# Performance work log

Measured on AMD Instinct MI355X. Metric: run time of the kernel, lower is better.

Reference implementation:

```python
import jax, jax.numpy as jnp
import numpy as np

N_VOCAB = 100000
N_FIELDS = 40
K = 64
ATTN = 64
BATCH = 2048

def setup_inputs() -> dict:
    key = jax.random.key(0)
    ks = jax.random.split(key, 9)
    x = jax.random.randint(ks[0], (BATCH, N_FIELDS), 0, N_VOCAB)
    lin_table = jax.random.normal(ks[1], (N_VOCAB, 1), dtype=jnp.float32) * 0.01
    V_table = jax.random.normal(ks[2], (N_VOCAB, K), dtype=jnp.float32) * 0.01
    W1 = jax.random.normal(ks[3], (K, ATTN), dtype=jnp.float32) * (1.0 / np.sqrt(K))
    b1 = jnp.zeros((ATTN,), dtype=jnp.float32)
    W2 = jax.random.normal(ks[4], (ATTN, 1), dtype=jnp.float32) * (1.0 / np.sqrt(ATTN))
    b2 = jnp.zeros((1,), dtype=jnp.float32)
    Wf = jax.random.normal(ks[5], (K, 1), dtype=jnp.float32) * (1.0 / np.sqrt(K))
    bf = jnp.zeros((1,), dtype=jnp.float32)
    return {"x": x, "lin_table": lin_table, "V_table": V_table,
            "W1": W1, "b1": b1, "W2": W2, "b2": b2, "Wf": Wf, "bf": bf}

def reference(x, lin_table, V_table, W1, b1, W2, b2, Wf, bf):
    # linear part: sum of per-feature scalar weights -> [B, 1]
    linear_part = jnp.sum(lin_table[x], axis=1)
    # embeddings: [B, F, K]
    embd = V_table[x]
    # pairwise interactions: [B, F, F, K]
    pw = embd[:, :, None, :] * embd[:, None, :, :]
    # attention MLP: k -> attn -> 1, scores [B, F, F, 1]
    h = jax.nn.relu(jnp.einsum('bijk,ka->bija', pw, W1) + b1)
    scores = jnp.einsum('bija,ao->bijo', h, W2) + b2
    # softmax over dim=2 (second field axis)
    probs = jax.nn.softmax(scores, axis=2)
    # weighted sum over j then i -> [B, K]
    weighted = jnp.sum(probs * pw, axis=2)
    weighted_embd = jnp.sum(weighted, axis=1)
    interaction_part = weighted_embd @ Wf + bf  # [B, 1]
    return jax.nn.sigmoid(linear_part + interaction_part)[:, 0]
```

## Files before the change

kernel.cpp:

```cpp
#include <hip/hip_runtime.h>

#define NF 40
#define KD 64

typedef float f32x4 __attribute__((ext_vector_type(4)));
typedef _Float16 f16x8 __attribute__((ext_vector_type(8)));
typedef _Float16 f16x4 __attribute__((ext_vector_type(4)));

__global__ __launch_bounds__(256, 4)
void afm_kernel(const int* __restrict__ x,
                const float* __restrict__ lin_table,
                const float* __restrict__ V_table,
                const float* __restrict__ W1,
                const float* __restrict__ b1,
                const float* __restrict__ W2,
                const float* __restrict__ b2,
                const float* __restrict__ Wf,
                const float* __restrict__ bf,
                float* __restrict__ out)
{
    __shared__ _Float16 e16[NF][72];
    __shared__ _Float16 eT16[KD][72];
    __shared__ _Float16 Q16[48][72];
    __shared__ unsigned short lut[832];
    __shared__ float wsum[4];

    const int b = blockIdx.x;
    const int tid = threadIdx.x;
    const int w = tid >> 6;
    const int lane = tid & 63;
    const int l15 = lane & 15;
    const int lhi = lane >> 4;

    {
        f16x8 zh = {0, 0, 0, 0, 0, 0, 0, 0};
        for (int t = tid; t < 48 * 72 / 8; t += 256)
            reinterpret_cast<f16x8*>(&Q16[0][0])[t] = zh;
        int r = tid >> 2, c8 = tid & 3;
        *reinterpret_cast<f16x8*>(&eT16[r][40 + 8 * c8]) = zh;
    }
    for (int p0 = tid; p0 < 832; p0 += 256) {
        int p = p0 > 819 ? 819 : p0;
        int i = (int)((81.0f - sqrtf(6561.0f - 8.0f * (float)p)) * 0.5f);
        int off = (i * (81 - i)) >> 1;
        if ((((i + 1) * (80 - i)) >> 1) <= p) { ++i; off = (i * (81 - i)) >> 1; }
        else if (off > p)                     { --i; off = (i * (81 - i)) >> 1; }
        lut[p0] = (unsigned short)((i << 8) | (i + (p - off)));
    }

    for (int q = tid; q < NF * (KD / 4); q += 256) {
        int i = q >> 4, k4 = q & 15;
        int ix = x[b * NF + i];
        float4 v = reinterpret_cast<const float4*>(V_table + (size_t)ix * KD)[k4];
        f16x4 hv = {(_Float16)v.x, (_Float16)v.y, (_Float16)v.z, (_Float16)v.w};
        *reinterpret_cast<f16x4*>(&e16[i][k4 * 4]) = hv;
        eT16[k4 * 4 + 0][i] = hv[0];
        eT16[k4 * 4 + 1][i] = hv[1];
        eT16[k4 * 4 + 2][i] = hv[2];
        eT16[k4 * 4 + 3][i] = hv[3];
    }
    float linv = (w == 0 && lane < NF) ? lin_table[x[b * NF + lane]] : 0.0f;

    f16x8 Af[4][2];
    #pragma unroll
    for (int at = 0; at < 4; ++at) {
        #pragma unroll
        for (int ks = 0; ks < 2; ++ks) {
            f16x8 t;
            #pragma unroll
            for (int el = 0; el < 8; ++el)
                t[el] = (_Float16)W1[(ks * 32 + lhi * 8 + el) * KD + at * 16 + l15];
            Af[at][ks] = t;
        }
    }
    f32x4 b1v[4], w2v[4];
    #pragma unroll
    for (int at = 0; at < 4; ++at) {
        b1v[at] = *reinterpret_cast<const f32x4*>(b1 + at * 16 + lhi * 4);
        w2v[at] = *reinterpret_cast<const f32x4*>(W2 + at * 16 + lhi * 4);
    }
    const float wfv = Wf[w * 16 + l15];
    const float bf0 = bf[0];
    __syncthreads();

    const int k0 = lhi * 8;
    for (int mt = w; mt < 52; mt += 4) {
        const int v = lut[mt * 16 + l15];
        const int i = v >> 8;
        const int j = v & 255;
        const _Float16* ei = &e16[i][0];
        const _Float16* ej = &e16[j][0];
        f16x8 B0 = (*reinterpret_cast<const f16x8*>(ei + k0)) *
                   (*reinterpret_cast<const f16x8*>(ej + k0));
        f16x8 B1 = (*reinterpret_cast<const f16x8*>(ei + k0 + 32)) *
                   (*reinterpret_cast<const f16x8*>(ej + k0 + 32));

        f32x4 d[4];
        #pragma unroll
        for (int at = 0; at < 4; ++at) {
            d[at] = b1v[at];
            d[at] = __builtin_amdgcn_mfma_f32_16x16x32_f16(Af[at][0], B0, d[at], 0, 0, 0);
            d[at] = __builtin_amdgcn_mfma_f32_16x16x32_f16(Af[at][1], B1, d[at], 0, 0, 0);
        }
        float s = 0.0f;
        #pragma unroll
        for (int at = 0; at < 4; ++at) {
            #pragma unroll
            for (int r = 0; r < 4; ++r)
                s = fmaf(fmaxf(d[at][r], 0.0f), w2v[at][r], s);
        }
        s += __shfl_xor(s, 16, 64);
        s += __shfl_xor(s, 32, 64);
        float qv = __expf(s);
        if (lhi == 0) {
            _Float16 qh = (_Float16)qv;
            Q16[i][j] = qh;
            Q16[j][i] = qh;
        }
    }
    __syncthreads();

    const int c = w * 16 + l15;
    const f16x8 bv0 = *reinterpret_cast<const f16x8*>(&eT16[c][lhi * 8]);
    const f16x8 bv1 = *reinterpret_cast<const f16x8*>(&eT16[c][32 + lhi * 8]);
    f16x8 one0, one1;
    #pragma unroll
    for (int el = 0; el < 8; ++el) {
        one0[el] = (_Float16)1.0f;
        one1[el] = (lhi == 0) ? (_Float16)1.0f : (_Float16)0.0f;
    }

    float acc = 0.0f;
    #pragma unroll
    for (int mt = 0; mt < 3; ++mt) {
        const _Float16* qrow = &Q16[mt * 16 + l15][0];
        f16x8 aq0 = *reinterpret_cast<const f16x8*>(qrow + lhi * 8);
        f16x8 aq1 = *reinterpret_cast<const f16x8*>(qrow + 32 + lhi * 8);

        f32x4 dz = {0.f, 0.f, 0.f, 0.f};
        dz = __builtin_amdgcn_mfma_f32_16x16x32_f16(aq0, one0, dz, 0, 0, 0);
        dz = __builtin_amdgcn_mfma_f32_16x16x32_f16(aq1, one1, dz, 0, 0, 0);

        f32x4 dq = {0.f, 0.f, 0.f, 0.f};
        dq = __builtin_amdgcn_mfma_f32_16x16x32_f16(aq0, bv0, dq, 0, 0, 0);
        dq = __builtin_amdgcn_mfma_f32_16x16x32_f16(aq1, bv1, dq, 0, 0, 0);

        f16x4 ev4 = *reinterpret_cast<const f16x4*>(&eT16[c][mt * 16 + lhi * 4]);
        #pragma unroll
        for (int r = 0; r < 4; ++r) {
            int ii = mt * 16 + lhi * 4 + r;
            float rz = (ii < NF) ? __builtin_amdgcn_rcpf(dz[r]) : 0.0f;
            acc = fmaf((float)ev4[r] * dq[r], rz, acc);
        }
    }

    acc += __shfl_xor(acc, 16, 64);
    acc += __shfl_xor(acc, 32, 64);
    float ip = acc * wfv;
    ip += __shfl_xor(ip, 1, 64);
    ip += __shfl_xor(ip, 2, 64);
    ip += __shfl_xor(ip, 4, 64);
    ip += __shfl_xor(ip, 8, 64);
    if (lane == 0) wsum[w] = ip;
    __syncthreads();

    if (w == 0) {
        linv += __shfl_xor(linv, 32, 64);
        linv += __shfl_xor(linv, 16, 64);
        linv += __shfl_xor(linv, 8, 64);
        linv += __shfl_xor(linv, 4, 64);
        linv += __shfl_xor(linv, 2, 64);
        linv += __shfl_xor(linv, 1, 64);
        if (lane == 0) {
            float z = linv + wsum[0] + wsum[1] + wsum[2] + wsum[3] + bf0;
            out[b] = 1.0f / (1.0f + __expf(-z));
        }
    }
}

extern "C" void kernel_launch(void* const* d_in, const int* in_sizes, int n_in,
                              void* d_out, int out_size, void* d_ws, size_t ws_size,
                              hipStream_t stream) {
    const int*   x         = (const int*)d_in[0];
    const float* lin_table = (const float*)d_in[1];
    const float* V_table   = (const float*)d_in[2];
    const float* W1        = (const float*)d_in[3];
    const float* b1        = (const float*)d_in[4];
    const float* W2        = (const float*)d_in[5];
    const float* b2        = (const float*)d_in[6];
    const float* Wf        = (const float*)d_in[7];
    const float* bf        = (const float*)d_in[8];
    float* out = (float*)d_out;

    const int batch = in_sizes[0] / NF;
    afm_kernel<<<batch, 256, 0, stream>>>(x, lin_table, V_table, W1, b1, W2, b2,
                                          Wf, bf, out);
}
```

Before: 32.61 us.

## Process two samples per block and overlap second gather with first scoring

```diff
diff --git a/kernel.cpp b/kernel.cpp
--- a/kernel.cpp
+++ b/kernel.cpp
@@ -19,25 +19,28 @@
                 const float* __restrict__ bf,
                 float* __restrict__ out)
 {
-    __shared__ _Float16 e16[NF][72];
-    __shared__ _Float16 eT16[KD][72];
+    __shared__ _Float16 eA[2][NF][72];
+    __shared__ _Float16 eT[2][KD][72];
     __shared__ _Float16 Q16[48][72];
     __shared__ unsigned short lut[832];
     __shared__ float wsum[4];
 
-    const int b = blockIdx.x;
     const int tid = threadIdx.x;
     const int w = tid >> 6;
     const int lane = tid & 63;
     const int l15 = lane & 15;
     const int lhi = lane >> 4;
+    const int s0 = blockIdx.x * 2;
+    const int s1 = s0 + 1;
 
     {
         f16x8 zh = {0, 0, 0, 0, 0, 0, 0, 0};
-        for (int t = tid; t < 48 * 72 / 8; t += 256)
+        for (int t = tid; t < 432; t += 256)
             reinterpret_cast<f16x8*>(&Q16[0][0])[t] = zh;
-        int r = tid >> 2, c8 = tid & 3;
-        *reinterpret_cast<f16x8*>(&eT16[r][40 + 8 * c8]) = zh;
+        for (int t = tid; t < 512; t += 256) {
+            int s = t >> 8, r = (t >> 2) & 63, c8 = t & 3;
+            *reinterpret_cast<f16x8*>(&eT[s][r][40 + 8 * c8]) = zh;
+        }
     }
     for (int p0 = tid; p0 < 832; p0 += 256) {
         int p = p0 > 819 ? 819 : p0;
@@ -48,18 +51,20 @@
         lut[p0] = (unsigned short)((i << 8) | (i + (p - off)));
     }
 
-    for (int q = tid; q < NF * (KD / 4); q += 256) {
-        int i = q >> 4, k4 = q & 15;
-        int ix = x[b * NF + i];
-        float4 v = reinterpret_cast<const float4*>(V_table + (size_t)ix * KD)[k4];
-        f16x4 hv = {(_Float16)v.x, (_Float16)v.y, (_Float16)v.z, (_Float16)v.w};
-        *reinterpret_cast<f16x4*>(&e16[i][k4 * 4]) = hv;
-        eT16[k4 * 4 + 0][i] = hv[0];
-        eT16[k4 * 4 + 1][i] = hv[1];
-        eT16[k4 * 4 + 2][i] = hv[2];
-        eT16[k4 * 4 + 3][i] = hv[3];
-    }
-    float linv = (w == 0 && lane < NF) ? lin_table[x[b * NF + lane]] : 0.0f;
+    auto gather = [&](int smp, int s) -> float {
+        for (int q = tid; q < NF * (KD / 4); q += 256) {
+            int i = q >> 4, k4 = q & 15;
+            int ix = x[smp * NF + i];
+            float4 v = reinterpret_cast<const float4*>(V_table + (size_t)ix * KD)[k4];
+            f16x4 hv = {(_Float16)v.x, (_Float16)v.y, (_Float16)v.z, (_Float16)v.w};
+            *reinterpret_cast<f16x4*>(&eA[s][i][k4 * 4]) = hv;
+            eT[s][k4 * 4 + 0][i] = hv[0];
+            eT[s][k4 * 4 + 1][i] = hv[1];
+            eT[s][k4 * 4 + 2][i] = hv[2];
+            eT[s][k4 * 4 + 3][i] = hv[3];
+        }
+        return (w == 0 && lane < NF) ? lin_table[x[smp * NF + lane]] : 0.0f;
+    };
 
     f16x8 Af[4][2];
     #pragma unroll
@@ -81,90 +86,88 @@
     }
     const float wfv = Wf[w * 16 + l15];
     const float bf0 = bf[0];
-    __syncthreads();
-
     const int k0 = lhi * 8;
-    for (int mt = w; mt < 52; mt += 4) {
-        const int v = lut[mt * 16 + l15];
-        const int i = v >> 8;
-        const int j = v & 255;
-        const _Float16* ei = &e16[i][0];
-        const _Float16* ej = &e16[j][0];
-        f16x8 B0 = (*reinterpret_cast<const f16x8*>(ei + k0)) *
-                   (*reinterpret_cast<const f16x8*>(ej + k0));
-        f16x8 B1 = (*reinterpret_cast<const f16x8*>(ei + k0 + 32)) *
-                   (*reinterpret_cast<const f16x8*>(ej + k0 + 32));
-
-        f32x4 d[4];
+
+    auto score = [&](int s) {
+        for (int mt = w; mt < 52; mt += 4) {
+            const int v = lut[mt * 16 + l15];
+            const int i = v >> 8;
+            const int j = v & 255;
+            const _Float16* ei = &eA[s][i][0];
+            const _Float16* ej = &eA[s][j][0];
+            f16x8 B0 = (*reinterpret_cast<const f16x8*>(ei + k0)) *
+                       (*reinterpret_cast<const f16x8*>(ej + k0));
+            f16x8 B1 = (*reinterpret_cast<const f16x8*>(ei + k0 + 32)) *
+                       (*reinterpret_cast<const f16x8*>(ej + k0 + 32));
+            f32x4 d[4];
+            #pragma unroll
+            for (int at = 0; at < 4; ++at) {
+                d[at] = b1v[at];
+                d[at] = __builtin_amdgcn_mfma_f32_16x16x32_f16(Af[at][0], B0, d[at], 0, 0, 0);
+                d[at] = __builtin_amdgcn_mfma_f32_16x16x32_f16(Af[at][1], B1, d[at], 0, 0, 0);
+            }
+            float sacc = 0.0f;
+            #pragma unroll
+            for (int at = 0; at < 4; ++at) {
+                #pragma unroll
+                for (int r = 0; r < 4; ++r)
+                    sacc = fmaf(fmaxf(d[at][r], 0.0f), w2v[at][r], sacc);
+            }
+            sacc += __shfl_xor(sacc, 16, 64);
+            sacc += __shfl_xor(sacc, 32, 64);
+            float qv = __expf(sacc);
+            if (lhi == 0) {
+                _Float16 qh = (_Float16)qv;
+                Q16[i][j] = qh;
+                Q16[j][i] = qh;
+            }
+        }
+    };
+
+    auto pv = [&](int s) {
+        const int c = w * 16 + l15;
+        const f16x8 bv0 = *reinterpret_cast<const f16x8*>(&eT[s][c][lhi * 8]);
+        const f16x8 bv1 = *reinterpret_cast<const f16x8*>(&eT[s][c][32 + lhi * 8]);
+        f16x8 one0, one1;
         #pragma unroll
-        for (int at = 0; at < 4; ++at) {
-            d[at] = b1v[at];
-            d[at] = __builtin_amdgcn_mfma_f32_16x16x32_f16(Af[at][0], B0, d[at], 0, 0, 0);
-            d[at] = __builtin_amdgcn_mfma_f32_16x16x32_f16(Af[at][1], B1, d[at], 0, 0, 0);
-        }
-        float s = 0.0f;
+        for (int el = 0; el < 8; ++el) {
+            one0[el] = (_Float16)1.0f;
+            one1[el] = (lhi == 0) ? (_Float16)1.0f : (_Float16)0.0f;
+        }
+        float acc = 0.0f;
         #pragma unroll
-        for (int at = 0; at < 4; ++at) {
-            #pragma unroll
-            for (int r = 0; r < 4; ++r)
-                s = fmaf(fmaxf(d[at][r], 0.0f), w2v[at][r], s);
-        }
-        s += __shfl_xor(s, 16, 64);
-        s += __shfl_xor(s, 32, 64);
-        float qv = __expf(s);
-        if (lhi == 0) {
-            _Float16 qh = (_Float16)qv;
-            Q16[i][j] = qh;
-            Q16[j][i] = qh;
-        }
-    }
-    __syncthreads();
-
-    const int c = w * 16 + l15;
-    const f16x8 bv0 = *reinterpret_cast<const f16x8*>(&eT16[c][lhi * 8]);
-    const f16x8 bv1 = *reinterpret_cast<const f16x8*>(&eT16[c][32 + lhi * 8]);
-    f16x8 one0, one1;
-    #pragma unroll
-    for (int el = 0; el < 8; ++el) {
-        one0[el] = (_Float16)1.0f;
-        one1[el] = (lhi == 0) ? (_Float16)1.0f : (_Float16)0.0f;
-    }
-
-    float acc = 0.0f;
-    #pragma unroll
-    for (int mt = 0; mt < 3; ++mt) {
-        const _Float16* qrow = &Q16[mt * 16 + l15][0];
-        f16x8 aq0 = *reinterpret_cast<const f16x8*>(qrow + lhi * 8);
-        f16x8 aq1 = *reinterpret_cast<const f16x8*>(qrow + 32 + lhi * 8);
-
-        f32x4 dz = {0.f, 0.f, 0.f, 0.f};
-        dz = __builtin_amdgcn_mfma_f32_16x16x32_f16(aq0, one0, dz, 0, 0, 0);
-        dz = __builtin_amdgcn_mfma_f32_16x16x32_f16(aq1, one1, dz, 0, 0, 0);
-
-        f32x4 dq = {0.f, 0.f, 0.f, 0.f};
-        dq = __builtin_amdgcn_mfma_f32_16x16x32_f16(aq0, bv0, dq, 0, 0, 0);
-        dq = __builtin_amdgcn_mfma_f32_16x16x32_f16(aq1, bv1, dq, 0, 0, 0);
-
-        f16x4 ev4 = *reinterpret_cast<const f16x4*>(&eT16[c][mt * 16 + lhi * 4]);
-        #pragma unroll
-        for (int r = 0; r < 4; ++r) {
-            int ii = mt * 16 + lhi * 4 + r;
-            float rz = (ii < NF) ? __builtin_amdgcn_rcpf(dz[r]) : 0.0f;
-            acc = fmaf((float)ev4[r] * dq[r], rz, acc);
-        }
-    }
-
-    acc += __shfl_xor(acc, 16, 64);
-    acc += __shfl_xor(acc, 32, 64);
-    float ip = acc * wfv;
-    ip += __shfl_xor(ip, 1, 64);
-    ip += __shfl_xor(ip, 2, 64);
-    ip += __shfl_xor(ip, 4, 64);
-    ip += __shfl_xor(ip, 8, 64);
-    if (lane == 0) wsum[w] = ip;
-    __syncthreads();
-
-    if (w == 0) {
+        for (int mt = 0; mt < 3; ++mt) {
+            const _Float16* qrow = &Q16[mt * 16 + l15][0];
+            f16x8 aq0 = *reinterpret_cast<const f16x8*>(qrow + lhi * 8);
+            f16x8 aq1 = *reinterpret_cast<const f16x8*>(qrow + 32 + lhi * 8);
+
+            f32x4 dz = {0.f, 0.f, 0.f, 0.f};
+            dz = __builtin_amdgcn_mfma_f32_16x16x32_f16(aq0, one0, dz, 0, 0, 0);
+            dz = __builtin_amdgcn_mfma_f32_16x16x32_f16(aq1, one1, dz, 0, 0, 0);
+
+            f32x4 dq = {0.f, 0.f, 0.f, 0.f};
+            dq = __builtin_amdgcn_mfma_f32_16x16x32_f16(aq0, bv0, dq, 0, 0, 0);
+            dq = __builtin_amdgcn_mfma_f32_16x16x32_f16(aq1, bv1, dq, 0, 0, 0);
+
+            f16x4 ev4 = *reinterpret_cast<const f16x4*>(&eT[s][c][mt * 16 + lhi * 4]);
+            #pragma unroll
+            for (int r = 0; r < 4; ++r) {
+                int ii = mt * 16 + lhi * 4 + r;
+                float rz = (ii < NF) ? __builtin_amdgcn_rcpf(dz[r]) : 0.0f;
+                acc = fmaf((float)ev4[r] * dq[r], rz, acc);
+            }
+        }
+        acc += __shfl_xor(acc, 16, 64);
+        acc += __shfl_xor(acc, 32, 64);
+        float ip = acc * wfv;
+        ip += __shfl_xor(ip, 1, 64);
+        ip += __shfl_xor(ip, 2, 64);
+        ip += __shfl_xor(ip, 4, 64);
+        ip += __shfl_xor(ip, 8, 64);
+        if (lane == 0) wsum[w] = ip;
+    };
+
+    auto out_write = [&](int smp, float linv) {
         linv += __shfl_xor(linv, 32, 64);
         linv += __shfl_xor(linv, 16, 64);
         linv += __shfl_xor(linv, 8, 64);
@@ -173,9 +176,27 @@
         linv += __shfl_xor(linv, 1, 64);
         if (lane == 0) {
             float z = linv + wsum[0] + wsum[1] + wsum[2] + wsum[3] + bf0;
-            out[b] = 1.0f / (1.0f + __expf(-z));
-        }
-    }
+            out[smp] = 1.0f / (1.0f + __expf(-z));
+        }
+    };
+
+    float linv0 = gather(s0, 0);
+    __syncthreads();
+
+    float linv1 = gather(s1, 1);
+    score(0);
+    __syncthreads();
+
+    pv(0);
+    __syncthreads();
+    if (w == 0) out_write(s0, linv0);
+
+    score(1);
+    __syncthreads();
+
+    pv(1);
+    __syncthreads();
+    if (w == 0) out_write(s1, linv1);
 }
 
 extern "C" void kernel_launch(void* const* d_in, const int* in_sizes, int n_in,
@@ -193,6 +214,6 @@
     float* out = (float*)d_out;
 
     const int batch = in_sizes[0] / NF;
-    afm_kernel<<<batch, 256, 0, stream>>>(x, lin_table, V_table, W1, b1, W2, b2,
-                                          Wf, bf, out);
+    afm_kernel<<<batch / 2, 256, 0, stream>>>(x, lin_table, V_table, W1, b1, W2,
+                                              b2, Wf, bf, out);
 }
```

Measured after the change: 32.85 us. Within noise of the previous version (+0.8%).
